# Kernel tuning notes

Hardware: AMD Instinct MI355X
Metric: run time of the kernel (lower is better)

The kernel has to match this reference:

```python
import jax, jax.numpy as jnp
import numpy as np

N, D, H, K, C = 4096, 512, 8, 10, 4
DH = D // H

def _ln(x, g, b, eps=1e-5):
    m = jnp.mean(x, axis=-1, keepdims=True)
    v = jnp.mean((x - m) ** 2, axis=-1, keepdims=True)
    return (x - m) / jnp.sqrt(v + eps) * g + b

def _branch(x, Wfc, bfc, lng, lnb, Wq, Wk, Wv, Wo, ng, nb):
    # FC + GELU projection of patch features [N, D]
    x = jax.nn.gelu(x @ Wfc + bfc, approximate=False)
    # TransLayer: pre-LN multi-head self-attention with residual, returns per-instance attn A [1, N]
    h = _ln(x, lng, lnb)
    q = (h @ Wq).reshape(N, H, DH)
    k = (h @ Wk).reshape(N, H, DH)
    v = (h @ Wv).reshape(N, H, DH)
    scores = jnp.einsum('nhd,mhd->hnm', q, k) / jnp.sqrt(jnp.float32(DH))  # [H,N,N]
    attn = jax.nn.softmax(scores, axis=-1)
    o = jnp.einsum('hnm,mhd->nhd', attn, v).reshape(N, D) @ Wo
    x = x + o
    A = attn.mean(axis=(0, 1))[None, :]  # [1, N] mean attention received per instance
    feats = _ln(x, ng, nb)               # self.norm
    # top-k / bottom-k selection by descending sort of A[0]
    order = jnp.argsort(-A[0])
    atte = feats[jnp.concatenate([order[:K], order[-K:]])]  # [2K, D]
    slide = feats.mean(axis=0, keepdims=True)               # [1, D]
    return A, atte, slide

def _contrast_loss(HEa, IHCa, logit_scale):
    scale = jnp.exp(logit_scale)
    hn = HEa / jnp.linalg.norm(HEa, axis=1, keepdims=True)
    inn = IHCa / jnp.linalg.norm(IHCa, axis=1, keepdims=True)
    L = scale * (hn @ inn.T)  # [2K, 2K]
    def _half(M):
        # vectorized over the original python loop over i in range(K)
        def f(i):
            p1 = jnp.concatenate([M[:K, i][:, None], M[:K, K:]], axis=1)   # [K, K+1], label 0
            p2 = jnp.concatenate([M[K:, K + i][:, None], M[K:, :K]], axis=1)
            l1 = -jax.nn.log_softmax(p1, axis=-1)[:, 0].mean()
            l2 = -jax.nn.log_softmax(p2, axis=-1)[:, 0].mean()
            return l1 + l2
        return jax.vmap(f)(jnp.arange(K)).sum()
    return (_half(L) + _half(L.T)) / (4.0 * K)

def setup_inputs() -> dict:
    key = jax.random.key(0)
    ks = jax.random.split(key, 40)
    w = lambda k, shape: jax.random.normal(k, shape, jnp.float32) * 0.02
    return {
        'HE_x': jax.random.normal(ks[0], (N, D), jnp.float32),
        'IHC_x': jax.random.normal(ks[1], (N, D), jnp.float32),
        'W_he_fc': w(ks[2], (D, D)), 'b_he_fc': jnp.zeros((D,), jnp.float32),
        'W_ihc_fc': w(ks[3], (D, D)), 'b_ihc_fc': jnp.zeros((D,), jnp.float32),
        'he_ln_g': jnp.ones((D,), jnp.float32), 'he_ln_b': jnp.zeros((D,), jnp.float32),
        'he_Wq': w(ks[4], (D, D)), 'he_Wk': w(ks[5], (D, D)), 'he_Wv': w(ks[6], (D, D)), 'he_Wo': w(ks[7], (D, D)),
        'ihc_ln_g': jnp.ones((D,), jnp.float32), 'ihc_ln_b': jnp.zeros((D,), jnp.float32),
        'ihc_Wq': w(ks[8], (D, D)), 'ihc_Wk': w(ks[9], (D, D)), 'ihc_Wv': w(ks[10], (D, D)), 'ihc_Wo': w(ks[11], (D, D)),
        'norm_g': jnp.ones((D,), jnp.float32), 'norm_b': jnp.zeros((D,), jnp.float32),
        'W_he_cls': w(ks[12], (D, C)), 'b_he_cls': jnp.zeros((C,), jnp.float32),
        'W_ihc_cls': w(ks[13], (D, C)), 'b_ihc_cls': jnp.zeros((C,), jnp.float32),
        'W_fc': w(ks[14], (2 * D, D)), 'b_fc': jnp.zeros((D,), jnp.float32),
        'W_c1': w(ks[15], (3 * D, D)), 'b_c1': jnp.zeros((D,), jnp.float32),
        'W_c2': w(ks[16], (D, C)), 'b_c2': jnp.zeros((C,), jnp.float32),
        'logit_scale': jnp.asarray(np.log(1.0 / 0.07), jnp.float32),
    }

def reference(HE_x, IHC_x, W_he_fc, b_he_fc, W_ihc_fc, b_ihc_fc,
              he_ln_g, he_ln_b, he_Wq, he_Wk, he_Wv, he_Wo,
              ihc_ln_g, ihc_ln_b, ihc_Wq, ihc_Wk, ihc_Wv, ihc_Wo,
              norm_g, norm_b, W_he_cls, b_he_cls, W_ihc_cls, b_ihc_cls,
              W_fc, b_fc, W_c1, b_c1, W_c2, b_c2, logit_scale):
    HE_A, HE_atte, HE_tok = _branch(HE_x, W_he_fc, b_he_fc, he_ln_g, he_ln_b,
                                    he_Wq, he_Wk, he_Wv, he_Wo, norm_g, norm_b)
    IHC_A, IHC_atte, IHC_tok = _branch(IHC_x, W_ihc_fc, b_ihc_fc, ihc_ln_g, ihc_ln_b,
                                       ihc_Wq, ihc_Wk, ihc_Wv, ihc_Wo, norm_g, norm_b)
    HE_logit = HE_tok @ W_he_cls + b_he_cls      # [1, C]
    IHC_logit = IHC_tok @ W_ihc_cls + b_ihc_cls  # [1, C]
    # TailFusion
    concat_tok = jnp.concatenate([HE_tok, IHC_tok], axis=-1) @ W_fc + b_fc
    fused = jnp.concatenate([HE_tok + IHC_tok, HE_tok * IHC_tok, concat_tok], axis=-1)
    MM_logit = jax.nn.gelu(fused @ W_c1 + b_c1, approximate=False) @ W_c2 + b_c2
    c_loss = _contrast_loss(HE_atte, IHC_atte, logit_scale)
    # pack result dict into one [4, C] array: rows = HE, IHC, MM logits, broadcast c_loss
    logits = jnp.concatenate([HE_logit, IHC_logit, MM_logit], axis=0)
    return jnp.concatenate([logits, jnp.full((1, C), c_loss, logits.dtype)], axis=0)
```

## Files before the change

kernel.cpp:

```cpp
#include <hip/hip_runtime.h>
#include <hip/hip_bf16.h>
#include <math.h>

#define DEV __device__ __forceinline__

typedef __attribute__((ext_vector_type(4))) float  f32x4;
typedef __attribute__((ext_vector_type(8))) short  bf8_t;
typedef unsigned int   u32;
typedef unsigned short u16;

DEV u16 f2bf(float f){
  u32 u = __builtin_bit_cast(u32, f);
  u32 r = (u + 0x7fffu + ((u >> 16) & 1u)) >> 16;
  return (u16)r;
}
DEV float bf2f(u16 h){ u32 u = ((u32)h) << 16; return __builtin_bit_cast(float, u); }
DEV u32 swzB(u32 r, u32 b, u32 rowBytes){ return r*rowBytes + (b ^ ((r & 7u) << 4)); }

DEV void gll16(const void* g, void* l){
  __builtin_amdgcn_global_load_lds(
      (const __attribute__((address_space(1))) unsigned int*)g,
      (__attribute__((address_space(3))) unsigned int*)l, 16, 0, 0);
}

#define EL2M 2097152
#define WBR  1310720

__global__ void k_split_w(
    const float* __restrict__ A0, const float* __restrict__ A1,
    const float* __restrict__ A2, const float* __restrict__ A3,
    const float* __restrict__ A4,
    const float* __restrict__ B0, const float* __restrict__ B1,
    const float* __restrict__ B2, const float* __restrict__ B3,
    const float* __restrict__ B4, u16* __restrict__ ob)
{
  const int which = blockIdx.y, br = blockIdx.z;
  const float* w = br ? ((which==0)?B0:(which==1)?B1:(which==2)?B2:(which==3)?B3:B4)
                      : ((which==0)?A0:(which==1)?A1:(which==2)?A2:(which==3)?A3:A4);
  int i = blockIdx.x*256 + threadIdx.x;
  int k = i >> 9, c = i & 511;
  u16* base = ob + (size_t)br*WBR;
  base[which*262144 + c*512 + k] = f2bf(w[i]);
}

__global__ __launch_bounds__(256) void k_ln(
    const float* __restrict__ xg, const float* __restrict__ g0, const float* __restrict__ b0,
    const float* __restrict__ g1, const float* __restrict__ b1, u16* __restrict__ shiB)
{
  const int br = blockIdx.y;
  const float* x = xg + (size_t)br*EL2M;
  const float* g = br ? g1 : g0;
  const float* b = br ? b1 : b0;
  u16* out = shiB + (size_t)br*EL2M;
  const int w = threadIdx.x >> 6, lane = threadIdx.x & 63;
  const int row = blockIdx.x*4 + w;
  const float* xr = x + row*512;
  float v[8];
  f32x4 a  = *(const f32x4*)(xr + lane*8);
  f32x4 a2 = *(const f32x4*)(xr + lane*8 + 4);
  v[0]=a.x; v[1]=a.y; v[2]=a.z; v[3]=a.w; v[4]=a2.x; v[5]=a2.y; v[6]=a2.z; v[7]=a2.w;
  float s = v[0]+v[1]+v[2]+v[3]+v[4]+v[5]+v[6]+v[7];
  #pragma unroll
  for (int m=1;m<64;m<<=1) s += __shfl_xor(s, m);
  const float mean = s * (1.0f/512.0f);
  float q = 0.f;
  #pragma unroll
  for (int i=0;i<8;++i){ const float d = v[i]-mean; q += d*d; }
  #pragma unroll
  for (int m=1;m<64;m<<=1) q += __shfl_xor(q, m);
  const float rstd = 1.0f / sqrtf(q*(1.0f/512.0f) + 1e-5f);
  #pragma unroll
  for (int i=0;i<8;++i){
    const int c = lane*8 + i;
    out[row*512 + c] = f2bf((v[i]-mean)*rstd*g[c] + b[c]);
  }
}

__global__ __launch_bounds__(256) void k_gemm_fc(
    const float* __restrict__ X0, const float* __restrict__ X1,
    const u16* __restrict__ wb,
    const float* __restrict__ b0, const float* __restrict__ b1,
    float* __restrict__ xgB)
{
  __shared__ __align__(16) char ls[16384];
  const int br = blockIdx.z;
  const float* X = br ? X1 : X0;
  const float* bias = br ? b1 : b0;
  const u16* Bthi = wb + (size_t)br*WBR;
  float* outF = xgB + (size_t)br*EL2M;
  const int t = threadIdx.x;
  const int w = t >> 6, lane = t & 63;
  const int n0 = blockIdx.x * 64;
  const int c0 = blockIdx.y * 64;
  const int wr = w >> 1, wc = w & 1;
  const int lr = lane & 15, lg = lane >> 4;

  auto stageB = [&](const u16* __restrict__ src, char* lbase, int row0, int kb){
    #pragma unroll
    for (int j=0;j<2;++j){
      const int ci = w*128 + j*64 + lane;
      const int r  = ci >> 3, cl = ci & 7;
      const int cs = cl ^ (r & 7);
      gll16(src + (size_t)(row0 + r)*512 + kb + cs*8, lbase + w*2048 + j*1024);
    }
  };

  f32x4 acc[2][2];
  #pragma unroll
  for (int i=0;i<2;++i)
    #pragma unroll
    for (int j=0;j<2;++j) acc[i][j] = f32x4{0.f,0.f,0.f,0.f};

  for (int bk = 0; bk < 8; ++bk) {
    const int kb = bk * 64;
    __syncthreads();
    stageB(Bthi, ls + 8192, c0, kb);
    #pragma unroll 4
    for (int i = t; i < 1024; i += 256) {
      const int r = i >> 4, c = i & 15;
      const f32x4 xv = *(const f32x4*)(X + (n0 + r)*512 + kb + c*4);
      u32 h01, h23;
      asm("v_cvt_pk_bf16_f32 %0, %1, %2" : "=v"(h01) : "v"(xv.x), "v"(xv.y));
      asm("v_cvt_pk_bf16_f32 %0, %1, %2" : "=v"(h23) : "v"(xv.z), "v"(xv.w));
      *(uint2*)(ls + swzB(r, c*8, 128)) = uint2{h01, h23};
    }
    __syncthreads();
    #pragma unroll
    for (int ks = 0; ks < 2; ++ks) {
      const u32 co = ks*64 + lg*16;
      bf8_t ah[2], bh[2];
      #pragma unroll
      for (int i=0;i<2;++i) {
        ah[i] = *(const bf8_t*)(ls +        swzB(wr*32 + i*16 + lr, co, 128));
        bh[i] = *(const bf8_t*)(ls + 8192 + swzB(wc*32 + i*16 + lr, co, 128));
      }
      #pragma unroll
      for (int i=0;i<2;++i)
        #pragma unroll
        for (int j=0;j<2;++j)
          acc[i][j] = __builtin_amdgcn_mfma_f32_16x16x32_bf16(ah[i], bh[j], acc[i][j], 0,0,0);
    }
  }
  #pragma unroll
  for (int i=0;i<2;++i)
    #pragma unroll
    for (int j=0;j<2;++j) {
      const int col = c0 + wc*32 + j*16 + lr;
      #pragma unroll
      for (int r=0;r<4;++r) {
        const int row = n0 + wr*32 + i*16 + lg*4 + r;
        float v = acc[i][j][r] + bias[col];
        outF[row*512 + col] = 0.5f * v * (1.0f + erff(v * 0.70710678118654752f));
      }
    }
}

__global__ __launch_bounds__(256) void k_gemm_qkv(
    const u16* __restrict__ shiB, const u16* __restrict__ wb,
    u16* __restrict__ qhB, u16* __restrict__ khB, u16* __restrict__ vTB)
{
  __shared__ __align__(16) char ls[16384];
  const int z = blockIdx.z;
  const int br = z / 3, which = z % 3;
  const u16* Ahi  = shiB + (size_t)br*EL2M;
  const u16* Bthi = wb + (size_t)br*WBR + (size_t)(1+which)*262144;
  const int t = threadIdx.x;
  const int w = t >> 6, lane = t & 63;
  const int n0 = blockIdx.x * 64;
  const int c0 = blockIdx.y * 64;
  const int wr = w >> 1, wc = w & 1;
  const int lr = lane & 15, lg = lane >> 4;

  auto stage = [&](const u16* __restrict__ src, char* lbase, int row0, int kb){
    #pragma unroll
    for (int j=0;j<2;++j){
      const int ci = w*128 + j*64 + lane;
      const int r  = ci >> 3, cl = ci & 7;
      const int cs = cl ^ (r & 7);
      gll16(src + (size_t)(row0 + r)*512 + kb + cs*8, lbase + w*2048 + j*1024);
    }
  };

  f32x4 acc[2][2];
  #pragma unroll
  for (int i=0;i<2;++i)
    #pragma unroll
    for (int j=0;j<2;++j) acc[i][j] = f32x4{0.f,0.f,0.f,0.f};

  for (int bk = 0; bk < 8; ++bk) {
    const int kb = bk * 64;
    __syncthreads();
    stage(Ahi,  ls,        n0, kb);
    stage(Bthi, ls + 8192, c0, kb);
    __syncthreads();
    #pragma unroll
    for (int ks = 0; ks < 2; ++ks) {
      const u32 co = ks*64 + lg*16;
      bf8_t ah[2], bh[2];
      #pragma unroll
      for (int i=0;i<2;++i) {
        ah[i] = *(const bf8_t*)(ls +        swzB(wr*32 + i*16 + lr, co, 128));
        bh[i] = *(const bf8_t*)(ls + 8192 + swzB(wc*32 + i*16 + lr, co, 128));
      }
      #pragma unroll
      for (int i=0;i<2;++i)
        #pragma unroll
        for (int j=0;j<2;++j)
          acc[i][j] = __builtin_amdgcn_mfma_f32_16x16x32_bf16(ah[i], bh[j], acc[i][j], 0,0,0);
    }
  }
  u16* outQ = qhB + (size_t)br*EL2M;
  u16* outK = khB + (size_t)br*EL2M;
  u16* outV = vTB + (size_t)br*EL2M;
  #pragma unroll
  for (int i=0;i<2;++i)
    #pragma unroll
    for (int j=0;j<2;++j) {
      const int col = c0 + wc*32 + j*16 + lr;
      #pragma unroll
      for (int r=0;r<4;++r) {
        const int row = n0 + wr*32 + i*16 + lg*4 + r;
        const u16 hv = f2bf(acc[i][j][r]);
        if (which == 2)      outV[(size_t)col*4096 + row] = hv;
        else if (which == 1) outK[row*512 + col] = hv;
        else                 outQ[row*512 + col] = hv;
      }
    }
}

__global__ __launch_bounds__(256) void k_attn(
    const u16* __restrict__ qhiB, const u16* __restrict__ khiB,
    const u16* __restrict__ vtB,  u16* __restrict__ ovB, float* __restrict__ ApartB)
{
  __shared__ __align__(16) char ls[32768];
  const int t = threadIdx.x, w = t >> 6, lane = t & 63;
  const int lr = lane & 15, lg = lane >> 4;
  const int bid = blockIdx.x;
  const int h = bid & 7, br = (bid >> 3) & 1, nb = bid >> 4;
  const int n0 = nb * 64, qc0 = h * 64;
  const u16* qhi = qhiB + (size_t)br*EL2M;
  const u16* khi = khiB + (size_t)br*EL2M;
  const u16* vt  = vtB  + (size_t)br*EL2M;
  u16* ov        = ovB  + (size_t)br*EL2M;
  float* Apart   = ApartB + (size_t)br*EL2M;
  const float cexp = 0.18033688011112042f;

  bf8_t qf[4][2];
  #pragma unroll
  for (int b=0;b<4;++b)
    #pragma unroll
    for (int ks=0;ks<2;++ks)
      qf[b][ks] = *(const bf8_t*)(qhi + (n0 + b*16 + lr)*512 + qc0 + ks*32 + lg*8);

  const u16* kbase = khi + (size_t)(w*32 + lr)*512 + qc0 + lg*8;
  const u16* vbase = vt + (size_t)(qc0 + w*16 + lr)*4096 + lg*8;

  auto loadK = [&](int mt, bf8_t (&kk)[2][2]){
    const u16* kb = kbase + (size_t)(mt*128)*512;
    #pragma unroll
    for (int ks=0;ks<2;++ks){
      kk[0][ks] = *(const bf8_t*)(kb + ks*32);
      kk[1][ks] = *(const bf8_t*)(kb + 16*512 + ks*32);
    }
  };
  auto loadV = [&](int mt, bf8_t (&vv)[4]){
    #pragma unroll
    for (int k2=0;k2<4;++k2) vv[k2] = *(const bf8_t*)(vbase + mt*128 + k2*32);
  };

  float rs[4] = {0.f,0.f,0.f,0.f};
  {
    bf8_t kA[2][2], kB[2][2];
    loadK(0, kA); loadK(1, kB);
    auto qkexp = [&](bf8_t (&kk)[2][2]){
      f32x4 sacc[2][4];
      #pragma unroll
      for (int a=0;a<2;++a)
        #pragma unroll
        for (int b=0;b<4;++b) sacc[a][b] = f32x4{0.f,0.f,0.f,0.f};
      #pragma unroll
      for (int ks=0;ks<2;++ks)
        #pragma unroll
        for (int b=0;b<4;++b){
          sacc[0][b] = __builtin_amdgcn_mfma_f32_16x16x32_bf16(kk[0][ks], qf[b][ks], sacc[0][b], 0,0,0);
          sacc[1][b] = __builtin_amdgcn_mfma_f32_16x16x32_bf16(kk[1][ks], qf[b][ks], sacc[1][b], 0,0,0);
        }
      #pragma unroll
      for (int a=0;a<2;++a)
        #pragma unroll
        for (int b=0;b<4;++b)
          #pragma unroll
          for (int r=0;r<4;++r)
            rs[b] += __builtin_amdgcn_exp2f(sacc[a][b][r] * cexp);
    };
    for (int mt = 0; mt < 32; mt += 2){
      qkexp(kA);
      if (mt+2 < 32) loadK(mt+2, kA);
      qkexp(kB);
      if (mt+3 < 32) loadK(mt+3, kB);
    }
  }
  #pragma unroll
  for (int b=0;b<4;++b){ rs[b] += __shfl_xor(rs[b],16); rs[b] += __shfl_xor(rs[b],32); }
  {
    float* red = (float*)ls;
    if (lg == 0){
      #pragma unroll
      for (int b=0;b<4;++b) red[w*64 + b*16 + lr] = rs[b];
    }
    __syncthreads();
    float* rinv = (float*)(ls + 1024);
    if (t < 64) rinv[t] = 1.0f / (red[t] + red[64+t] + red[128+t] + red[192+t]);
    __syncthreads();
  }
  float lrv[4];
  #pragma unroll
  for (int b=0;b<4;++b) lrv[b] = log2f(((const float*)(ls + 1024))[b*16 + lr]);
  __syncthreads();

  f32x4 oacc[4];
  #pragma unroll
  for (int i=0;i<4;++i) oacc[i] = f32x4{0.f,0.f,0.f,0.f};
  {
    bf8_t kA[2][2], kB[2][2], vA[4], vB[4];
    loadK(0, kA); loadV(0, vA);
    loadK(1, kB); loadV(1, vB);
    auto step2 = [&](int mt, bf8_t (&kk)[2][2], bf8_t (&vv)[4], u32 pb){
      const int m0 = mt * 128;
      f32x4 sacc[2][4];
      #pragma unroll
      for (int a=0;a<2;++a)
        #pragma unroll
        for (int b=0;b<4;++b) sacc[a][b] = f32x4{0.f,0.f,0.f,0.f};
      #pragma unroll
      for (int ks=0;ks<2;++ks)
        #pragma unroll
        for (int b=0;b<4;++b){
          sacc[0][b] = __builtin_amdgcn_mfma_f32_16x16x32_bf16(kk[0][ks], qf[b][ks], sacc[0][b], 0,0,0);
          sacc[1][b] = __builtin_amdgcn_mfma_f32_16x16x32_bf16(kk[1][ks], qf[b][ks], sacc[1][b], 0,0,0);
        }
      if (mt+2 < 32) loadK(mt+2, kk);
      float cs[2][4];
      #pragma unroll
      for (int a=0;a<2;++a){ cs[a][0]=0.f; cs[a][1]=0.f; cs[a][2]=0.f; cs[a][3]=0.f; }
      #pragma unroll
      for (int a=0;a<2;++a){
        const u32 mbyte = (w*32 + a*16 + lg*4)*2;
        #pragma unroll
        for (int b=0;b<4;++b){
          const float p0 = __builtin_amdgcn_exp2f(sacc[a][b][0]*cexp + lrv[b]);
          const float p1 = __builtin_amdgcn_exp2f(sacc[a][b][1]*cexp + lrv[b]);
          const float p2 = __builtin_amdgcn_exp2f(sacc[a][b][2]*cexp + lrv[b]);
          const float p3 = __builtin_amdgcn_exp2f(sacc[a][b][3]*cexp + lrv[b]);
          cs[a][0]+=p0; cs[a][1]+=p1; cs[a][2]+=p2; cs[a][3]+=p3;
          u32 u01, u23;
          asm("v_cvt_pk_bf16_f32 %0, %1, %2" : "=v"(u01) : "v"(p0), "v"(p1));
          asm("v_cvt_pk_bf16_f32 %0, %1, %2" : "=v"(u23) : "v"(p2), "v"(p3));
          *(uint2*)(ls + pb + swzB(b*16 + lr, mbyte, 256)) = uint2{u01, u23};
        }
      }
      #pragma unroll
      for (int a=0;a<2;++a)
        #pragma unroll
        for (int r=0;r<4;++r){
          float v = cs[a][r];
          v += __shfl_xor(v,1); v += __shfl_xor(v,2);
          v += __shfl_xor(v,4); v += __shfl_xor(v,8);
          cs[a][r] = v;
        }
      if (lr == 0){
        const int base = (h*64 + nb)*4096 + m0 + w*32;
        #pragma unroll
        for (int a=0;a<2;++a)
          #pragma unroll
          for (int r=0;r<4;++r)
            Apart[base + a*16 + lg*4 + r] = cs[a][r];
      }
      __syncthreads();
      #pragma unroll
      for (int ks2 = 0; ks2 < 4; ++ks2) {
        const u32 co = ks2*64 + lg*16;
        #pragma unroll
        for (int i=0;i<4;++i){
          const bf8_t ap = *(const bf8_t*)(ls + pb + swzB(i*16 + lr, co, 256));
          oacc[i] = __builtin_amdgcn_mfma_f32_16x16x32_bf16(ap, vv[ks2], oacc[i], 0,0,0);
        }
      }
      if (mt+2 < 32) loadV(mt+2, vv);
    };
    for (int mt = 0; mt < 32; mt += 2){
      step2(mt,   kA, vA, 0);
      step2(mt+1, kB, vB, 16384);
    }
  }
  #pragma unroll
  for (int i=0;i<4;++i)
    #pragma unroll
    for (int r=0;r<4;++r){
      const int row = n0 + i*16 + lg*4 + r;
      const int col = qc0 + w*16 + lr;
      ov[row*512 + col] = f2bf(oacc[i][r]);
    }
}

__global__ void k_reduceA1(const float* __restrict__ ApartB, double* __restrict__ A64p){
  const int br = blockIdx.z;
  const float* Apart = ApartB + (size_t)br*EL2M;
  const int m = blockIdx.x*256 + threadIdx.x;
  const int kb = blockIdx.y;
  double s = 0.0;
  for (int b = kb*64; b < kb*64 + 64; ++b) s += (double)Apart[b*4096 + m];
  A64p[br*32768 + kb*4096 + m] = s;
}
__global__ void k_reduceA2(const double* __restrict__ A64p, double* __restrict__ A64){
  const int br = blockIdx.y;
  const int m = blockIdx.x*256 + threadIdx.x;
  double s = 0.0;
  #pragma unroll
  for (int kb=0;kb<8;++kb) s += A64p[br*32768 + kb*4096 + m];
  A64[br*4096 + m] = s;
}

__global__ __launch_bounds__(256) void k_select(const double* __restrict__ A64B, int* __restrict__ idxB){
  __shared__ double Aw[4096];
  __shared__ double wv_[4];
  __shared__ int    wi_[4];
  const double* A64 = A64B + (size_t)blockIdx.x*4096;
  int* idx = idxB + blockIdx.x*32;
  const int t = threadIdx.x, w = t >> 6, lane = t & 63;
  for (int i=t;i<4096;i+=256) Aw[i] = A64[i];
  __syncthreads();
  for (int k=0;k<10;++k){
    double best = -1e300; int bidx = 1<<30;
    for (int i=t;i<4096;i+=256){
      const double v = Aw[i];
      if (v > best){ best = v; bidx = i; }
    }
    #pragma unroll
    for (int m=1;m<64;m<<=1){
      const double ovv = __shfl_xor(best, m);
      const int    oii = __shfl_xor(bidx, m);
      if (ovv > best || (ovv == best && oii < bidx)){ best = ovv; bidx = oii; }
    }
    if (lane == 0){ wv_[w] = best; wi_[w] = bidx; }
    __syncthreads();
    if (t == 0){
      double bb = wv_[0]; int bi2 = wi_[0];
      #pragma unroll
      for (int q=1;q<4;++q)
        if (wv_[q] > bb || (wv_[q] == bb && wi_[q] < bi2)){ bb = wv_[q]; bi2 = wi_[q]; }
      idx[k] = bi2; Aw[bi2] = -1e300;
    }
    __syncthreads();
  }
  for (int i=t;i<4096;i+=256) Aw[i] = A64[i];
  __syncthreads();
  for (int k=0;k<10;++k){
    double best = 1e300; int bidx = -1;
    for (int i=t;i<4096;i+=256){
      const double v = Aw[i];
      if (v < best || (v == best && i > bidx)){ best = v; bidx = i; }
    }
    #pragma unroll
    for (int m=1;m<64;m<<=1){
      const double ovv = __shfl_xor(best, m);
      const int    oii = __shfl_xor(bidx, m);
      if (ovv < best || (ovv == best && oii > bidx)){ best = ovv; bidx = oii; }
    }
    if (lane == 0){ wv_[w] = best; wi_[w] = bidx; }
    __syncthreads();
    if (t == 0){
      double bb = wv_[0]; int bi2 = wi_[0];
      #pragma unroll
      for (int q=1;q<4;++q)
        if (wv_[q] < bb || (wv_[q] == bb && wi_[q] > bi2)){ bb = wv_[q]; bi2 = wi_[q]; }
      idx[19-k] = bi2; Aw[bi2] = 1e300;
    }
    __syncthreads();
  }
}

__global__ __launch_bounds__(256) void k_gemm_wo(
    const u16* __restrict__ ovB, const u16* __restrict__ wb,
    const float* __restrict__ xgB, float* __restrict__ AXB)
{
  __shared__ __align__(16) char ls[16384];
  const int br = blockIdx.z;
  const u16* Ahi  = ovB + (size_t)br*EL2M;
  const u16* Bthi = wb + (size_t)br*WBR + 4*262144;
  const float* resid = xgB + (size_t)br*EL2M;
  float* outF = AXB + (size_t)br*EL2M;
  const int t = threadIdx.x;
  const int w = t >> 6, lane = t & 63;
  const int n0 = blockIdx.x * 64;
  const int c0 = blockIdx.y * 64;
  const int wr = w >> 1, wc = w & 1;
  const int lr = lane & 15, lg = lane >> 4;

  auto stage = [&](const u16* __restrict__ src, char* lbase, int row0, int kb){
    #pragma unroll
    for (int j=0;j<2;++j){
      const int ci = w*128 + j*64 + lane;
      const int r  = ci >> 3, cl = ci & 7;
      const int cs = cl ^ (r & 7);
      gll16(src + (size_t)(row0 + r)*512 + kb + cs*8, lbase + w*2048 + j*1024);
    }
  };

  f32x4 acc[2][2];
  #pragma unroll
  for (int i=0;i<2;++i)
    #pragma unroll
    for (int j=0;j<2;++j) acc[i][j] = f32x4{0.f,0.f,0.f,0.f};

  for (int bk = 0; bk < 8; ++bk) {
    const int kb = bk * 64;
    __syncthreads();
    stage(Ahi,  ls,        n0, kb);
    stage(Bthi, ls + 8192, c0, kb);
    __syncthreads();
    #pragma unroll
    for (int ks = 0; ks < 2; ++ks) {
      const u32 co = ks*64 + lg*16;
      bf8_t ah[2], bh[2];
      #pragma unroll
      for (int i=0;i<2;++i) {
        ah[i] = *(const bf8_t*)(ls +        swzB(wr*32 + i*16 + lr, co, 128));
        bh[i] = *(const bf8_t*)(ls + 8192 + swzB(wc*32 + i*16 + lr, co, 128));
      }
      #pragma unroll
      for (int i=0;i<2;++i)
        #pragma unroll
        for (int j=0;j<2;++j)
          acc[i][j] = __builtin_amdgcn_mfma_f32_16x16x32_bf16(ah[i], bh[j], acc[i][j], 0,0,0);
    }
  }
  #pragma unroll
  for (int i=0;i<2;++i)
    #pragma unroll
    for (int j=0;j<2;++j) {
      const int col = c0 + wc*32 + j*16 + lr;
      #pragma unroll
      for (int r=0;r<4;++r) {
        const int row = n0 + wr*32 + i*16 + lg*4 + r;
        outF[row*512 + col] = acc[i][j][r] + resid[row*512 + col];
      }
    }
}

__global__ __launch_bounds__(256) void k_slide_part(const float* __restrict__ AXB,
                                                    float* __restrict__ spartB){
  __shared__ float acc[4][512];
  const int br = blockIdx.y;
  const float* xres = AXB + (size_t)br*EL2M;
  float* spart = spartB + (size_t)br*32768;
  const int t = threadIdx.x, w = t >> 6, lane = t & 63;
  float la[8];
  #pragma unroll
  for (int i=0;i<8;++i) la[i]=0.f;
  for (int rr = 0; rr < 16; ++rr) {
    const int row = blockIdx.x*64 + w*16 + rr;
    const float* xr = xres + row*512;
    float v[8];
    f32x4 a  = *(const f32x4*)(xr + lane*8);
    f32x4 a2 = *(const f32x4*)(xr + lane*8 + 4);
    v[0]=a.x; v[1]=a.y; v[2]=a.z; v[3]=a.w; v[4]=a2.x; v[5]=a2.y; v[6]=a2.z; v[7]=a2.w;
    float s = v[0]+v[1]+v[2]+v[3]+v[4]+v[5]+v[6]+v[7];
    #pragma unroll
    for (int m=1;m<64;m<<=1) s += __shfl_xor(s, m);
    const float mean = s * (1.0f/512.0f);
    float q = 0.f;
    #pragma unroll
    for (int i=0;i<8;++i){ const float d = v[i]-mean; q += d*d; }
    #pragma unroll
    for (int m=1;m<64;m<<=1) q += __shfl_xor(q, m);
    const float rstd = 1.0f / sqrtf(q*(1.0f/512.0f) + 1e-5f);
    #pragma unroll
    for (int i=0;i<8;++i) la[i] += (v[i]-mean)*rstd;
  }
  #pragma unroll
  for (int i=0;i<8;++i) acc[w][lane*8+i] = la[i];
  __syncthreads();
  for (int c = t; c < 512; c += 256)
    spart[blockIdx.x*512 + c] = acc[0][c]+acc[1][c]+acc[2][c]+acc[3][c];
}

__global__ void k_slide_reduce(const float* __restrict__ spartB, const float* __restrict__ g,
                               const float* __restrict__ b, float* __restrict__ tokB){
  const int br = blockIdx.y;
  const float* spart = spartB + (size_t)br*32768;
  const int c = blockIdx.x*256 + threadIdx.x;
  float s = 0.f;
  for (int bb=0;bb<64;++bb) s += spart[bb*512 + c];
  tokB[br*512 + c] = g[c]*(s*(1.0f/4096.0f)) + b[c];
}

__global__ void k_atte(const float* __restrict__ AXB, const int* __restrict__ idxB,
                       const float* __restrict__ g, const float* __restrict__ b,
                       float* __restrict__ atteB){
  const int br = blockIdx.y;
  const int i = blockIdx.x, lane = threadIdx.x;
  const int row = idxB[br*32 + i];
  const float* xr = AXB + (size_t)br*EL2M + row*512;
  float v[8];
  f32x4 a  = *(const f32x4*)(xr + lane*8);
  f32x4 a2 = *(const f32x4*)(xr + lane*8 + 4);
  v[0]=a.x; v[1]=a.y; v[2]=a.z; v[3]=a.w; v[4]=a2.x; v[5]=a2.y; v[6]=a2.z; v[7]=a2.w;
  float s = v[0]+v[1]+v[2]+v[3]+v[4]+v[5]+v[6]+v[7];
  #pragma unroll
  for (int m=1;m<64;m<<=1) s += __shfl_xor(s, m);
  const float mean = s * (1.0f/512.0f);
  float q = 0.f;
  #pragma unroll
  for (int i2=0;i2<8;++i2){ const float d = v[i2]-mean; q += d*d; }
  #pragma unroll
  for (int m=1;m<64;m<<=1) q += __shfl_xor(q, m);
  const float rstd = 1.0f / sqrtf(q*(1.0f/512.0f) + 1e-5f);
  #pragma unroll
  for (int i2=0;i2<8;++i2){
    const int c = lane*8 + i2;
    atteB[br*10240 + i*512 + c] = (v[i2]-mean)*rstd*g[c] + b[c];
  }
}

__global__ __launch_bounds__(256) void k_fused_part(
    const float* __restrict__ tokB, const float* __restrict__ Wfc2,
    float* __restrict__ partF)
{
  __shared__ float part[8][32];
  const int t = threadIdx.x, jj = t & 31, rg = t >> 5;
  const int j = blockIdx.x*32 + jj;
  const int r0 = blockIdx.y*128;
  float s = 0.f;
  #pragma unroll 4
  for (int i = 0; i < 16; ++i){
    const int r = r0 + rg + i*8;
    s += tokB[r] * Wfc2[r*512 + j];
  }
  part[rg][jj] = s;
  __syncthreads();
  if (t < 32){
    float acc = 0.f;
    #pragma unroll
    for (int g=0; g<8; ++g) acc += part[g][t];
    partF[blockIdx.y*512 + blockIdx.x*32 + t] = acc;
  }
}

__global__ void k_fused_fin(
    const float* __restrict__ tokB, const float* __restrict__ partF,
    const float* __restrict__ bfc2, float* __restrict__ fused)
{
  const int j = blockIdx.x*256 + threadIdx.x;
  float acc = bfc2[j];
  #pragma unroll
  for (int kb=0;kb<8;++kb) acc += partF[kb*512 + j];
  const float hv = tokB[j], iv = tokB[512 + j];
  fused[j]        = hv + iv;
  fused[512 + j]  = hv * iv;
  fused[1024 + j] = acc;
}

__global__ __launch_bounds__(256) void k_g1_part(
    const float* __restrict__ fused, const float* __restrict__ Wc1,
    float* __restrict__ partG)
{
  __shared__ float part[8][32];
  const int t = threadIdx.x, jj = t & 31, rg = t >> 5;
  const int j = blockIdx.x*32 + jj;
  const int r0 = blockIdx.y*128;
  float s = 0.f;
  #pragma unroll 4
  for (int i = 0; i < 16; ++i){
    const int r = r0 + rg + i*8;
    s += fused[r] * Wc1[r*512 + j];
  }
  part[rg][jj] = s;
  __syncthreads();
  if (t < 32){
    float acc = 0.f;
    #pragma unroll
    for (int g=0; g<8; ++g) acc += part[g][t];
    partG[blockIdx.y*512 + blockIdx.x*32 + t] = acc;
  }
}

__global__ void k_g1_fin(const float* __restrict__ partG, const float* __restrict__ bc1,
                         float* __restrict__ g1)
{
  const int j = blockIdx.x*256 + threadIdx.x;
  float acc = bc1[j];
  #pragma unroll
  for (int kb=0;kb<12;++kb) acc += partG[kb*512 + j];
  g1[j] = 0.5f*acc*(1.0f + erff(acc*0.70710678118654752f));
}

__global__ __launch_bounds__(256) void k_lm(
    const float* __restrict__ atteB, const float* __restrict__ lscale, float* __restrict__ Lm)
{
  __shared__ float ra[512];
  __shared__ float nAs;
  const float* atteH = atteB;
  const float* atteI = atteB + 10240;
  const int a = blockIdx.x, t = threadIdx.x, w = t >> 6, l = t & 63;
  for (int i=t;i<512;i+=256) ra[i] = atteH[a*512+i];
  __syncthreads();
  if (w == 0){
    float s = 0.f;
    #pragma unroll
    for (int k=0;k<8;++k){ const float v = ra[l + k*64]; s += v*v; }
    #pragma unroll
    for (int m=1;m<64;m<<=1) s += __shfl_xor(s, m);
    if (l == 0) nAs = s;
  }
  __syncthreads();
  const float scale = expf(lscale[0]);
  const float nA = sqrtf(nAs);
  for (int bi = 0; bi < 5; ++bi){
    const int b = w + bi*4;
    float dot = 0.f, nb = 0.f;
    #pragma unroll
    for (int k=0;k<8;++k){
      const float vb = atteI[b*512 + l + k*64];
      dot += ra[l + k*64]*vb;
      nb  += vb*vb;
    }
    #pragma unroll
    for (int m=1;m<64;m<<=1){ dot += __shfl_xor(dot,m); nb += __shfl_xor(nb,m); }
    if (l == 0) Lm[a*20 + b] = scale * dot / (nA * sqrtf(nb));
  }
}

__global__ __launch_bounds__(256) void k_loss(
    const float* __restrict__ tokB, const float* __restrict__ g1G, const float* __restrict__ LmG,
    const float* __restrict__ WheC, const float* __restrict__ bheC,
    const float* __restrict__ WihcC, const float* __restrict__ bihcC,
    const float* __restrict__ Wc2, const float* __restrict__ bc2,
    float* __restrict__ out)
{
  __shared__ float sH[512], sI[512], g1[512];
  __shared__ float Lm[20][20];
  __shared__ double terms[512];
  const int t = threadIdx.x, w = t >> 6, l = t & 63;
  for (int i=t;i<512;i+=256){ sH[i]=tokB[i]; sI[i]=tokB[512+i]; g1[i]=g1G[i]; }
  for (int i=t;i<400;i+=256) ((float*)Lm)[i] = LmG[i];
  __syncthreads();
  if (w < 3){
    const float* x  = (w==0)? sH   : (w==1)? sI    : g1;
    const float* W  = (w==0)? WheC : (w==1)? WihcC : Wc2;
    const float* bb = (w==0)? bheC : (w==1)? bihcC : bc2;
    const int c = l & 3, rg = l >> 2;
    float s = 0.f;
    for (int r = rg; r < 512; r += 16) s += x[r]*W[r*4+c];
    #pragma unroll
    for (int m=4;m<64;m<<=1) s += __shfl_xor(s, m);
    if (rg == 0) out[w*4 + c] = s + bb[c];
  }
  for (int e=t;e<512;e+=256){
    double res = 0.0;
    if (e < 400){
      const int r = e % 10, part = (e/10) % 2, i2 = (e/20) % 10, half = e/200;
      const int a = part ? (10 + r) : r;
      const int c0 = part ? (10 + i2) : i2;
      const int qb = part ? 0 : 10;
      auto Mget = [&](int aa, int bb)->double{
        return (double)(half ? Lm[bb][aa] : Lm[aa][bb]);
      };
      const double v0 = Mget(a, c0);
      double mx = v0;
      #pragma unroll
      for (int q=0;q<10;++q){ const double v = Mget(a, qb+q); if (v > mx) mx = v; }
      double se = exp(v0 - mx);
      #pragma unroll
      for (int q=0;q<10;++q) se += exp(Mget(a, qb+q) - mx);
      res = (log(se) + mx) - v0;
    }
    terms[e] = res;
  }
  __syncthreads();
  for (int s2=256;s2>0;s2>>=1){
    if (t < s2) terms[t] += terms[t+s2];
    __syncthreads();
  }
  if (t == 0) {
    const float cl = (float)(terms[0] / 400.0);
    out[12]=cl; out[13]=cl; out[14]=cl; out[15]=cl;
  }
}

extern "C" void kernel_launch(void* const* d_in, const int* in_sizes, int n_in,
                              void* d_out, int out_size, void* d_ws, size_t ws_size,
                              hipStream_t stream)
{
  (void)in_sizes; (void)n_in; (void)out_size; (void)ws_size;
  auto F = [&](int i){ return (const float*)d_in[i]; };
  char* ws = (char*)d_ws;
  size_t off = 0;
  auto alloc = [&](size_t sz)->void*{ void* p = ws + off; off += (sz + 255) & ~((size_t)255); return p; };

  float* xg   = (float*)alloc((size_t)2*EL2M*4);
  float* AX   = (float*)alloc((size_t)2*EL2M*4);
  u16*   shi  = (u16*)alloc((size_t)2*EL2M*2);
  u16*   qh   = (u16*)alloc((size_t)2*EL2M*2);
  u16*   kh   = (u16*)alloc((size_t)2*EL2M*2);
  u16*   vT   = (u16*)alloc((size_t)2*EL2M*2);
  u16*   ov   = (u16*)alloc((size_t)2*EL2M*2);
  u16*   wb   = (u16*)alloc((size_t)2*WBR*2);
  double* A64p= (double*)alloc((size_t)2*32768*8);
  double* A64 = (double*)alloc((size_t)2*4096*8);
  int*   idxB = (int*)alloc(2*32*4);
  float* spart= (float*)alloc((size_t)2*32768*4);
  float* tokB = (float*)alloc(2*512*4);
  float* attB = (float*)alloc((size_t)2*10240*4);
  float* fusedW = (float*)alloc(1536*4);
  float* g1W    = (float*)alloc(512*4);
  float* LmW    = (float*)alloc(400*4);
  float* partF  = (float*)alloc((size_t)8*512*4);
  float* partG  = (float*)alloc((size_t)12*512*4);

  k_split_w<<<dim3(1024,5,2),256,0,stream>>>(
      F(2),F(8),F(9),F(10),F(11),
      F(4),F(14),F(15),F(16),F(17),
      wb);
  k_gemm_fc<<<dim3(64,8,2),256,0,stream>>>(F(0), F(1), wb, F(3), F(5), xg);
  k_ln<<<dim3(1024,2),256,0,stream>>>(xg, F(6), F(7), F(12), F(13), shi);
  k_gemm_qkv<<<dim3(64,8,6),256,0,stream>>>(shi, wb, qh, kh, vT);
  k_attn<<<1024,256,0,stream>>>(qh, kh, vT, ov, AX);
  k_reduceA1<<<dim3(16,8,2),256,0,stream>>>(AX, A64p);
  k_reduceA2<<<dim3(16,2),256,0,stream>>>(A64p, A64);
  k_select<<<2,256,0,stream>>>(A64, idxB);
  k_gemm_wo<<<dim3(64,8,2),256,0,stream>>>(ov, wb, xg, AX);
  k_slide_part<<<dim3(64,2),256,0,stream>>>(AX, spart);
  k_slide_reduce<<<dim3(2,2),256,0,stream>>>(spart, F(18), F(19), tokB);
  k_atte<<<dim3(20,2),64,0,stream>>>(AX, idxB, F(18), F(19), attB);

  k_fused_part<<<dim3(16,8),256,0,stream>>>(tokB, F(24), partF);
  k_fused_fin<<<2,256,0,stream>>>(tokB, partF, F(25), fusedW);
  k_g1_part<<<dim3(16,12),256,0,stream>>>(fusedW, F(26), partG);
  k_g1_fin<<<2,256,0,stream>>>(partG, F(27), g1W);
  k_lm<<<20,256,0,stream>>>(attB, F(30), LmW);
  k_loss<<<1,256,0,stream>>>(tokB, g1W, LmW,
                             F(20), F(21), F(22), F(23), F(28), F(29),
                             (float*)d_out);
}
```

Measured before the change: 379.9 us.

## Move PV accumulation into first attention pass with deferred row normalization

The first pass of the attention kernel now computes unnormalized exp scores, writes them as bf16 to LDS and accumulates P·V there, while also summing row totals. The output is normalized at the end by the reciprocal row sum. The second pass only recomputes normalized probabilities for the column sums of A and no longer stages through LDS or runs the PV MFMAs, so it loses a per-tile barrier. The LDS tile switches from an XOR swizzle to a padded row stride, and the first pass gains barriers and V loads, so the work moves between passes rather than disappearing. Skipping max subtraction is safe only while the scores stay small enough for bf16 exponentials.

```diff
diff --git a/kernel.cpp b/kernel.cpp
--- a/kernel.cpp
+++ b/kernel.cpp
@@ -25,6 +25,8 @@
 
 #define EL2M 2097152
 #define WBR  1310720
+#define PSTR 272
+#define P1OFF 17408
 
 __global__ void k_split_w(
     const float* __restrict__ A0, const float* __restrict__ A1,
@@ -232,7 +234,7 @@
     const u16* __restrict__ qhiB, const u16* __restrict__ khiB,
     const u16* __restrict__ vtB,  u16* __restrict__ ovB, float* __restrict__ ApartB)
 {
-  __shared__ __align__(16) char ls[32768];
+  __shared__ __align__(16) char ls[34816];
   const int t = threadIdx.x, w = t >> 6, lane = t & 63;
   const int lr = lane & 15, lg = lane >> 4;
   const int bid = blockIdx.x;
@@ -268,11 +270,15 @@
     for (int k2=0;k2<4;++k2) vv[k2] = *(const bf8_t*)(vbase + mt*128 + k2*32);
   };
 
+  f32x4 oacc[4];
+  #pragma unroll
+  for (int i=0;i<4;++i) oacc[i] = f32x4{0.f,0.f,0.f,0.f};
   float rs[4] = {0.f,0.f,0.f,0.f};
   {
-    bf8_t kA[2][2], kB[2][2];
-    loadK(0, kA); loadK(1, kB);
-    auto qkexp = [&](bf8_t (&kk)[2][2]){
+    bf8_t kA[2][2], kB[2][2], vA[4], vB[4];
+    loadK(0, kA); loadV(0, vA);
+    loadK(1, kB); loadV(1, vB);
+    auto stepA = [&](int mt, bf8_t (&kk)[2][2], bf8_t (&vv)[4], u32 pb){
       f32x4 sacc[2][4];
       #pragma unroll
       for (int a=0;a<2;++a)
@@ -285,23 +291,44 @@
           sacc[0][b] = __builtin_amdgcn_mfma_f32_16x16x32_bf16(kk[0][ks], qf[b][ks], sacc[0][b], 0,0,0);
           sacc[1][b] = __builtin_amdgcn_mfma_f32_16x16x32_bf16(kk[1][ks], qf[b][ks], sacc[1][b], 0,0,0);
         }
-      #pragma unroll
-      for (int a=0;a<2;++a)
-        #pragma unroll
-        for (int b=0;b<4;++b)
-          #pragma unroll
-          for (int r=0;r<4;++r)
-            rs[b] += __builtin_amdgcn_exp2f(sacc[a][b][r] * cexp);
+      if (mt+2 < 32) loadK(mt+2, kk);
+      #pragma unroll
+      for (int a=0;a<2;++a){
+        const u32 mb = w*64 + a*32 + lg*8;
+        #pragma unroll
+        for (int b=0;b<4;++b){
+          const float e0 = __builtin_amdgcn_exp2f(sacc[a][b][0]*cexp);
+          const float e1 = __builtin_amdgcn_exp2f(sacc[a][b][1]*cexp);
+          const float e2 = __builtin_amdgcn_exp2f(sacc[a][b][2]*cexp);
+          const float e3 = __builtin_amdgcn_exp2f(sacc[a][b][3]*cexp);
+          rs[b] += (e0+e1)+(e2+e3);
+          u32 u01, u23;
+          asm("v_cvt_pk_bf16_f32 %0, %1, %2" : "=v"(u01) : "v"(e0), "v"(e1));
+          asm("v_cvt_pk_bf16_f32 %0, %1, %2" : "=v"(u23) : "v"(e2), "v"(e3));
+          *(uint2*)(ls + pb + (u32)(b*16 + lr)*PSTR + mb) = uint2{u01, u23};
+        }
+      }
+      __syncthreads();
+      #pragma unroll
+      for (int ks2 = 0; ks2 < 4; ++ks2) {
+        const u32 co = ks2*64 + lg*16;
+        #pragma unroll
+        for (int i=0;i<4;++i){
+          const bf8_t ap = *(const bf8_t*)(ls + pb + (u32)(i*16 + lr)*PSTR + co);
+          oacc[i] = __builtin_amdgcn_mfma_f32_16x16x32_bf16(ap, vv[ks2], oacc[i], 0,0,0);
+        }
+      }
+      if (mt+2 < 32) loadV(mt+2, vv);
     };
     for (int mt = 0; mt < 32; mt += 2){
-      qkexp(kA);
-      if (mt+2 < 32) loadK(mt+2, kA);
-      qkexp(kB);
-      if (mt+3 < 32) loadK(mt+3, kB);
-    }
-  }
+      stepA(mt,   kA, vA, 0);
+      stepA(mt+1, kB, vB, P1OFF);
+    }
+  }
+
   #pragma unroll
   for (int b=0;b<4;++b){ rs[b] += __shfl_xor(rs[b],16); rs[b] += __shfl_xor(rs[b],32); }
+  __syncthreads();
   {
     float* red = (float*)ls;
     if (lg == 0){
@@ -316,17 +343,11 @@
   float lrv[4];
   #pragma unroll
   for (int b=0;b<4;++b) lrv[b] = log2f(((const float*)(ls + 1024))[b*16 + lr]);
-  __syncthreads();
-
-  f32x4 oacc[4];
-  #pragma unroll
-  for (int i=0;i<4;++i) oacc[i] = f32x4{0.f,0.f,0.f,0.f};
+
   {
-    bf8_t kA[2][2], kB[2][2], vA[4], vB[4];
-    loadK(0, kA); loadV(0, vA);
-    loadK(1, kB); loadV(1, vB);
-    auto step2 = [&](int mt, bf8_t (&kk)[2][2], bf8_t (&vv)[4], u32 pb){
-      const int m0 = mt * 128;
+    bf8_t kA[2][2], kB[2][2];
+    loadK(0, kA); loadK(1, kB);
+    auto stepB = [&](int mt, bf8_t (&kk)[2][2]){
       f32x4 sacc[2][4];
       #pragma unroll
       for (int a=0;a<2;++a)
@@ -344,21 +365,14 @@
       #pragma unroll
       for (int a=0;a<2;++a){ cs[a][0]=0.f; cs[a][1]=0.f; cs[a][2]=0.f; cs[a][3]=0.f; }
       #pragma unroll
-      for (int a=0;a<2;++a){
-        const u32 mbyte = (w*32 + a*16 + lg*4)*2;
+      for (int a=0;a<2;++a)
         #pragma unroll
         for (int b=0;b<4;++b){
-          const float p0 = __builtin_amdgcn_exp2f(sacc[a][b][0]*cexp + lrv[b]);
-          const float p1 = __builtin_amdgcn_exp2f(sacc[a][b][1]*cexp + lrv[b]);
-          const float p2 = __builtin_amdgcn_exp2f(sacc[a][b][2]*cexp + lrv[b]);
-          const float p3 = __builtin_amdgcn_exp2f(sacc[a][b][3]*cexp + lrv[b]);
-          cs[a][0]+=p0; cs[a][1]+=p1; cs[a][2]+=p2; cs[a][3]+=p3;
-          u32 u01, u23;
-          asm("v_cvt_pk_bf16_f32 %0, %1, %2" : "=v"(u01) : "v"(p0), "v"(p1));
-          asm("v_cvt_pk_bf16_f32 %0, %1, %2" : "=v"(u23) : "v"(p2), "v"(p3));
-          *(uint2*)(ls + pb + swzB(b*16 + lr, mbyte, 256)) = uint2{u01, u23};
+          cs[a][0] += __builtin_amdgcn_exp2f(sacc[a][b][0]*cexp + lrv[b]);
+          cs[a][1] += __builtin_amdgcn_exp2f(sacc[a][b][1]*cexp + lrv[b]);
+          cs[a][2] += __builtin_amdgcn_exp2f(sacc[a][b][2]*cexp + lrv[b]);
+          cs[a][3] += __builtin_amdgcn_exp2f(sacc[a][b][3]*cexp + lrv[b]);
         }
-      }
       #pragma unroll
       for (int a=0;a<2;++a)
         #pragma unroll
@@ -369,37 +383,29 @@
           cs[a][r] = v;
         }
       if (lr == 0){
-        const int base = (h*64 + nb)*4096 + m0 + w*32;
+        const int base = (h*64 + nb)*4096 + mt*128 + w*32;
         #pragma unroll
         for (int a=0;a<2;++a)
           #pragma unroll
           for (int r=0;r<4;++r)
             Apart[base + a*16 + lg*4 + r] = cs[a][r];
       }
-      __syncthreads();
-      #pragma unroll
-      for (int ks2 = 0; ks2 < 4; ++ks2) {
-        const u32 co = ks2*64 + lg*16;
-        #pragma unroll
-        for (int i=0;i<4;++i){
-          const bf8_t ap = *(const bf8_t*)(ls + pb + swzB(i*16 + lr, co, 256));
-          oacc[i] = __builtin_amdgcn_mfma_f32_16x16x32_bf16(ap, vv[ks2], oacc[i], 0,0,0);
-        }
-      }
-      if (mt+2 < 32) loadV(mt+2, vv);
     };
     for (int mt = 0; mt < 32; mt += 2){
-      step2(mt,   kA, vA, 0);
-      step2(mt+1, kB, vB, 16384);
-    }
-  }
+      stepB(mt,   kA);
+      stepB(mt+1, kB);
+    }
+  }
+
+  const float* rinv = (const float*)(ls + 1024);
   #pragma unroll
   for (int i=0;i<4;++i)
     #pragma unroll
     for (int r=0;r<4;++r){
-      const int row = n0 + i*16 + lg*4 + r;
+      const int nl = i*16 + lg*4 + r;
+      const int row = n0 + nl;
       const int col = qc0 + w*16 + lr;
-      ov[row*512 + col] = f2bf(oacc[i][r]);
+      ov[row*512 + col] = f2bf(oacc[i][r] * rinv[nl]);
     }
 }
 
```

After: 385.5 us. Within noise of the previous version (+1.5%).
